# Performance work log

Hardware: AMD Instinct MI355X
Metric: run time of the kernel (lower is better)

The kernel has to match this reference:

```python
import jax, jax.numpy as jnp
import numpy as np

FEATURE_HEIGHT = 50
FEATURE_WIDTH = 50


def setup_inputs() -> dict:
    key = jax.random.key(0)
    k1, k2, k3 = jax.random.split(key, 3)
    bs, K, H, D = 16, FEATURE_HEIGHT * FEATURE_WIDTH, 8, 32
    Q, L, P = 2000, 1, 4
    value = jax.random.normal(k1, (bs, K, H, D), dtype=jnp.float32)
    value_spatial_shapes = jnp.array([[FEATURE_HEIGHT, FEATURE_WIDTH]], dtype=jnp.int64)
    sampling_locations = jax.random.uniform(k2, (bs, Q, H, L, P, 2), dtype=jnp.float32)
    attention_weights = jax.random.uniform(k3, (bs, Q, H, L, P), dtype=jnp.float32)
    return {
        "value": value,
        "value_spatial_shapes": value_spatial_shapes,
        "sampling_locations": sampling_locations,
        "attention_weights": attention_weights,
    }


def _bilinear_sample(img, grid):
    """torch.F.grid_sample(mode='bilinear', padding_mode='zeros', align_corners=False).

    img:  (N, D, h, w)
    grid: (N, Q, P, 2), last dim (x, y) in [-1, 1]
    returns (N, D, Q, P)
    """
    N, D, h, w = img.shape
    # unnormalize (align_corners=False)
    x = (grid[..., 0] + 1.0) * (w * 0.5) - 0.5  # (N, Q, P)
    y = (grid[..., 1] + 1.0) * (h * 0.5) - 0.5
    x0 = jnp.floor(x)
    y0 = jnp.floor(y)
    x1 = x0 + 1.0
    y1 = y0 + 1.0
    wx1 = x - x0
    wx0 = 1.0 - wx1
    wy1 = y - y0
    wy0 = 1.0 - wy1

    img_flat = img.reshape(N, D, h * w)

    def corner(ix, iy, wgt):
        valid = ((ix >= 0) & (ix < w) & (iy >= 0) & (iy < h)).astype(img.dtype)
        ixc = jnp.clip(ix, 0, w - 1).astype(jnp.int32)
        iyc = jnp.clip(iy, 0, h - 1).astype(jnp.int32)
        idx = (iyc * w + ixc).reshape(N, -1)  # (N, Q*P)
        vals = jnp.take_along_axis(img_flat, idx[:, None, :], axis=2)  # (N, D, Q*P)
        vals = vals.reshape(N, D, *ix.shape[1:])  # (N, D, Q, P)
        return vals * (wgt * valid)[:, None]

    out = corner(x0, y0, wx0 * wy0)
    out = out + corner(x1, y0, wx1 * wy0)
    out = out + corner(x0, y1, wx0 * wy1)
    out = out + corner(x1, y1, wx1 * wy1)
    return out


def reference(value, value_spatial_shapes, sampling_locations, attention_weights):
    bs, K, H, D = value.shape
    _, Q, _, L, P, _ = sampling_locations.shape
    h, w = FEATURE_HEIGHT, FEATURE_WIDTH

    sampling_grids = 2.0 * sampling_locations - 1.0  # (bs, Q, H, L, P, 2)
    # value -> (bs*H, D, h, w)
    v = value.reshape(bs, K, H * D).transpose(0, 2, 1).reshape(bs * H, D, h, w)
    # level 0 grid -> (bs*H, Q, P, 2)
    g = jnp.transpose(sampling_grids[:, :, :, 0], (0, 2, 1, 3, 4)).reshape(bs * H, Q, P, 2)
    sampled = _bilinear_sample(v, g)  # (bs*H, D, Q, P)
    # attention weights -> (bs*H, 1, Q, L*P)
    aw = jnp.transpose(attention_weights, (0, 2, 1, 3, 4)).reshape(bs * H, 1, Q, L * P)
    out = (sampled * aw).sum(-1)  # (bs*H, D, Q)
    out = out.reshape(bs, H * D, Q).transpose(0, 2, 1)  # (bs, Q, H*D)
    return out
```

## Files before the change

kernel.cpp:

```cpp
#include <hip/hip_runtime.h>


#define FH 50
#define FW 50
#define KK (FH * FW)
#define NH 8
#define ND 32
#define NQ 2000
#define NP 4
#define TPB 1024
#define QSLOTS (TPB / 4)
#define NPASS ((NQ + QSLOTS - 1) / QSLOTS)

typedef float f32x4 __attribute__((ext_vector_type(4)));

__global__ __launch_bounds__(TPB, 4) void deform_attn_kernel(
    const float* __restrict__ value,
    const float* __restrict__ loc,
    const float* __restrict__ attw,
    float* __restrict__ out)
{
    const int id = blockIdx.x;
    const int half = id >> 7;
    const int bh = id & 127;
    const int b  = bh >> 3;
    const int h  = bh & 7;

    __shared__ f32x4 lds[KK * 4];

    const int t = threadIdx.x;

    {
        const f32x4* __restrict__ src =
            (const f32x4*)value + (size_t)b * KK * 64 + h * 8 + half * 4;
#pragma unroll
        for (int i = 0; i < (KK * 4 + TPB - 1) / TPB; ++i) {
            const int idx = i * TPB + t;
            if (idx < KK * 4) {
                const int k = idx >> 2;
                const int q = idx & 3;
                lds[idx] = src[(size_t)k * 64 + q];
            }
        }
    }
    __syncthreads();

    const int quad = t & 3;
    const int qi = t >> 2;

    const f32x4* __restrict__ lp = (const f32x4*)loc;
    const f32x4* __restrict__ ap = (const f32x4*)attw;
    f32x4* __restrict__ op = (f32x4*)out;

    for (int pass = 0; pass < NPASS; ++pass) {
        const int qq = pass * QSLOTS + qi;
        if (qq >= NQ) break;

        const int gid = (b * NQ + qq) * NH + h;
        const f32x4 l0 = lp[(size_t)gid * 2 + 0];
        const f32x4 l1 = lp[(size_t)gid * 2 + 1];
        const f32x4 a4 = ap[gid];

        const float pxx[NP] = {l0.x, l0.z, l1.x, l1.z};
        const float pyy[NP] = {l0.y, l0.w, l1.y, l1.w};
        const float awp[NP] = {a4.x, a4.y, a4.z, a4.w};

        int   idx[16];
        float wts[16];
#pragma unroll
        for (int p = 0; p < NP; ++p) {
            const float fx = pxx[p] * (float)FW - 0.5f;
            const float fy = pyy[p] * (float)FH - 0.5f;
            const float x0f = floorf(fx);
            const float y0f = floorf(fy);
            const int x0 = (int)x0f, y0 = (int)y0f;
            const int x1 = x0 + 1, y1 = y0 + 1;
            const float wx1 = fx - x0f, wx0 = 1.f - wx1;
            const float wy1 = fy - y0f, wy0 = 1.f - wy1;

            const bool vx0 = (x0 >= 0) & (x0 < FW);
            const bool vx1 = (x1 >= 0) & (x1 < FW);
            const bool vy0 = (y0 >= 0) & (y0 < FH);
            const bool vy1 = (y1 >= 0) & (y1 < FH);

            const int cx0 = min(max(x0, 0), FW - 1);
            const int cx1 = min(max(x1, 0), FW - 1);
            const int cy0 = min(max(y0, 0), FH - 1);
            const int cy1 = min(max(y1, 0), FH - 1);

            idx[p * 4 + 0] = cy0 * FW + cx0;
            idx[p * 4 + 1] = cy0 * FW + cx1;
            idx[p * 4 + 2] = cy1 * FW + cx0;
            idx[p * 4 + 3] = cy1 * FW + cx1;

            wts[p * 4 + 0] = ((vx0 & vy0) ? (wx0 * wy0) : 0.f) * awp[p];
            wts[p * 4 + 1] = ((vx1 & vy0) ? (wx1 * wy0) : 0.f) * awp[p];
            wts[p * 4 + 2] = ((vx0 & vy1) ? (wx0 * wy1) : 0.f) * awp[p];
            wts[p * 4 + 3] = ((vx1 & vy1) ? (wx1 * wy1) : 0.f) * awp[p];
        }

        f32x4 acc = {0.f, 0.f, 0.f, 0.f};
#pragma unroll
        for (int i = 0; i < 16; ++i) {
            const f32x4 v = lds[idx[i] * 4 + quad];
            acc.x += wts[i] * v.x;
            acc.y += wts[i] * v.y;
            acc.z += wts[i] * v.z;
            acc.w += wts[i] * v.w;
        }

        op[(size_t)(b * NQ + qq) * 64 + h * 8 + half * 4 + quad] = acc;
    }
}

extern "C" void kernel_launch(void* const* d_in, const int* in_sizes, int n_in,
                              void* d_out, int out_size, void* d_ws, size_t ws_size,
                              hipStream_t stream) {
    const float* value = (const float*)d_in[0];
    const float* loc  = (const float*)d_in[2];
    const float* attw = (const float*)d_in[3];
    float* out = (float*)d_out;

    const int blocks = 2 * 16 * 8;
    deform_attn_kernel<<<blocks, TPB, 0, stream>>>(value, loc, attw, out);
}
```

Baseline: 115.6 us.

## Software-pipeline query loads and weight computation ahead of LDS gathers

```diff
diff --git a/kernel.cpp b/kernel.cpp
--- a/kernel.cpp
+++ b/kernel.cpp
@@ -10,7 +10,7 @@
 #define NP 4
 #define TPB 1024
 #define QSLOTS (TPB / 4)
-#define NPASS ((NQ + QSLOTS - 1) / QSLOTS)
+#define NPASS 8
 
 typedef float f32x4 __attribute__((ext_vector_type(4)));
 
@@ -29,44 +29,35 @@
     __shared__ f32x4 lds[KK * 4];
 
     const int t = threadIdx.x;
+    const int quad = t & 3;
+    const int qi = t >> 2;
+
+    const f32x4* __restrict__ lp = (const f32x4*)loc;
+    const f32x4* __restrict__ ap = (const f32x4*)attw;
+
+    const int gid0 = (b * NQ + qi) * NH + h;
+    f32x4 nl0 = lp[(size_t)gid0 * 2 + 0];
+    f32x4 nl1 = lp[(size_t)gid0 * 2 + 1];
+    f32x4 na  = ap[gid0];
 
     {
         const f32x4* __restrict__ src =
             (const f32x4*)value + (size_t)b * KK * 64 + h * 8 + half * 4;
 #pragma unroll
-        for (int i = 0; i < (KK * 4 + TPB - 1) / TPB; ++i) {
-            const int idx = i * TPB + t;
-            if (idx < KK * 4) {
-                const int k = idx >> 2;
-                const int q = idx & 3;
-                lds[idx] = src[(size_t)k * 64 + q];
-            }
+        for (int i = 0; i < 10; ++i) {
+            const int j = i * TPB + t;
+            if (j < KK * 4)
+                lds[j] = src[(size_t)(j >> 2) * 64 + (j & 3)];
         }
     }
-    __syncthreads();
 
-    const int quad = t & 3;
-    const int qi = t >> 2;
+    int   idx[16];
+    float wts[16];
 
-    const f32x4* __restrict__ lp = (const f32x4*)loc;
-    const f32x4* __restrict__ ap = (const f32x4*)attw;
-    f32x4* __restrict__ op = (f32x4*)out;
-
-    for (int pass = 0; pass < NPASS; ++pass) {
-        const int qq = pass * QSLOTS + qi;
-        if (qq >= NQ) break;
-
-        const int gid = (b * NQ + qq) * NH + h;
-        const f32x4 l0 = lp[(size_t)gid * 2 + 0];
-        const f32x4 l1 = lp[(size_t)gid * 2 + 1];
-        const f32x4 a4 = ap[gid];
-
+    auto computeOW = [&](const f32x4 l0, const f32x4 l1, const f32x4 a4) {
         const float pxx[NP] = {l0.x, l0.z, l1.x, l1.z};
         const float pyy[NP] = {l0.y, l0.w, l1.y, l1.w};
         const float awp[NP] = {a4.x, a4.y, a4.z, a4.w};
-
-        int   idx[16];
-        float wts[16];
 #pragma unroll
         for (int p = 0; p < NP; ++p) {
             const float fx = pxx[p] * (float)FW - 0.5f;
@@ -98,18 +89,56 @@
             wts[p * 4 + 2] = ((vx0 & vy1) ? (wx0 * wy1) : 0.f) * awp[p];
             wts[p * 4 + 3] = ((vx1 & vy1) ? (wx1 * wy1) : 0.f) * awp[p];
         }
+    };
 
-        f32x4 acc = {0.f, 0.f, 0.f, 0.f};
+    {
+        const f32x4 cl0 = nl0, cl1 = nl1, ca = na;
+        const int qn = qi + QSLOTS;
+        const int gidn = (b * NQ + qn) * NH + h;
+        nl0 = lp[(size_t)gidn * 2 + 0];
+        nl1 = lp[(size_t)gidn * 2 + 1];
+        na  = ap[gidn];
+        computeOW(cl0, cl1, ca);
+    }
+
+    __syncthreads();
+
+    f32x4* __restrict__ op = (f32x4*)out;
+
+#pragma unroll 1
+    for (int pass = 0; pass < NPASS; ++pass) {
+        const int qq = pass * QSLOTS + qi;
+
+        if (qq < NQ) {
+            f32x4 v[16];
 #pragma unroll
-        for (int i = 0; i < 16; ++i) {
-            const f32x4 v = lds[idx[i] * 4 + quad];
-            acc.x += wts[i] * v.x;
-            acc.y += wts[i] * v.y;
-            acc.z += wts[i] * v.z;
-            acc.w += wts[i] * v.w;
+            for (int i = 0; i < 16; ++i)
+                v[i] = lds[idx[i] * 4 + quad];
+            asm volatile("" ::
+                "v"(v[0]), "v"(v[1]), "v"(v[2]), "v"(v[3]),
+                "v"(v[4]), "v"(v[5]), "v"(v[6]), "v"(v[7]),
+                "v"(v[8]), "v"(v[9]), "v"(v[10]), "v"(v[11]),
+                "v"(v[12]), "v"(v[13]), "v"(v[14]), "v"(v[15]));
+            f32x4 acc = {0.f, 0.f, 0.f, 0.f};
+#pragma unroll
+            for (int i = 0; i < 16; ++i) {
+                acc.x += wts[i] * v[i].x;
+                acc.y += wts[i] * v[i].y;
+                acc.z += wts[i] * v[i].z;
+                acc.w += wts[i] * v[i].w;
+            }
+            op[(size_t)(b * NQ + qq) * 64 + h * 8 + half * 4 + quad] = acc;
         }
 
-        op[(size_t)(b * NQ + qq) * 64 + h * 8 + half * 4 + quad] = acc;
+        if (pass < NPASS - 1) {
+            const f32x4 cl0 = nl0, cl1 = nl1, ca = na;
+            const int qn = min(qq + 2 * QSLOTS, NQ - 1);
+            const int gidn = (b * NQ + qn) * NH + h;
+            nl0 = lp[(size_t)gidn * 2 + 0];
+            nl1 = lp[(size_t)gidn * 2 + 1];
+            na  = ap[gidn];
+            computeOW(cl0, cl1, ca);
+        }
     }
 }
 
```

Result: no change. 117.5 us (+1.7%).

## Map one query per thread with swizzled LDS, prefetch locations, XCD-aware block order

Applied to the files above, without the earlier changes.

```diff
diff --git a/kernel.cpp b/kernel.cpp
--- a/kernel.cpp
+++ b/kernel.cpp
@@ -9,10 +9,12 @@
 #define NQ 2000
 #define NP 4
 #define TPB 1024
-#define QSLOTS (TPB / 4)
-#define NPASS ((NQ + QSLOTS - 1) / QSLOTS)
 
 typedef float f32x4 __attribute__((ext_vector_type(4)));
+
+__device__ __forceinline__ int swz16(int k, int q) {
+    return (k << 2) ^ (q ^ (k & 3)) ^ (k & 4);
+}
 
 __global__ __launch_bounds__(TPB, 4) void deform_attn_kernel(
     const float* __restrict__ value,
@@ -20,53 +22,53 @@
     const float* __restrict__ attw,
     float* __restrict__ out)
 {
-    const int id = blockIdx.x;
-    const int half = id >> 7;
-    const int bh = id & 127;
-    const int b  = bh >> 3;
-    const int h  = bh & 7;
+    const int n = blockIdx.x;
+    const int xcd = n & 7;
+    const int slot = n >> 3;
+    const int b = xcd + ((slot >> 4) << 3);
+    const int rem = slot & 15;
+    const int h = rem >> 1;
+    const int half = rem & 1;
 
     __shared__ f32x4 lds[KK * 4];
 
     const int t = threadIdx.x;
 
+    const f32x4* __restrict__ lp = (const f32x4*)loc;
+    const f32x4* __restrict__ ap = (const f32x4*)attw;
+
+    const int gid0 = (b * NQ + t) * NH + h;
+    f32x4 l0A = lp[(size_t)gid0 * 2 + 0];
+    f32x4 l1A = lp[(size_t)gid0 * 2 + 1];
+    f32x4 aA  = ap[gid0];
+
     {
         const f32x4* __restrict__ src =
             (const f32x4*)value + (size_t)b * KK * 64 + h * 8 + half * 4;
 #pragma unroll
-        for (int i = 0; i < (KK * 4 + TPB - 1) / TPB; ++i) {
-            const int idx = i * TPB + t;
-            if (idx < KK * 4) {
-                const int k = idx >> 2;
-                const int q = idx & 3;
-                lds[idx] = src[(size_t)k * 64 + q];
+        for (int i = 0; i < 10; ++i) {
+            const int j = i * TPB + t;
+            if (j < KK * 4) {
+                const int k = j >> 2, q = j & 3;
+                lds[swz16(k, q)] = src[(size_t)k * 64 + q];
             }
         }
     }
-    __syncthreads();
 
-    const int quad = t & 3;
-    const int qi = t >> 2;
+    const int q1 = TPB + t;
+    const bool act1 = (q1 < NQ);
+    const int gid1 = (b * NQ + min(q1, NQ - 1)) * NH + h;
+    f32x4 l0B = lp[(size_t)gid1 * 2 + 0];
+    f32x4 l1B = lp[(size_t)gid1 * 2 + 1];
+    f32x4 aB  = ap[gid1];
 
-    const f32x4* __restrict__ lp = (const f32x4*)loc;
-    const f32x4* __restrict__ ap = (const f32x4*)attw;
-    f32x4* __restrict__ op = (f32x4*)out;
+    int   a16[16];
+    float wts[16];
 
-    for (int pass = 0; pass < NPASS; ++pass) {
-        const int qq = pass * QSLOTS + qi;
-        if (qq >= NQ) break;
-
-        const int gid = (b * NQ + qq) * NH + h;
-        const f32x4 l0 = lp[(size_t)gid * 2 + 0];
-        const f32x4 l1 = lp[(size_t)gid * 2 + 1];
-        const f32x4 a4 = ap[gid];
-
+    auto computeOW = [&](const f32x4 l0, const f32x4 l1, const f32x4 a4) {
         const float pxx[NP] = {l0.x, l0.z, l1.x, l1.z};
         const float pyy[NP] = {l0.y, l0.w, l1.y, l1.w};
         const float awp[NP] = {a4.x, a4.y, a4.z, a4.w};
-
-        int   idx[16];
-        float wts[16];
 #pragma unroll
         for (int p = 0; p < NP; ++p) {
             const float fx = pxx[p] * (float)FW - 0.5f;
@@ -88,28 +90,60 @@
             const int cy0 = min(max(y0, 0), FH - 1);
             const int cy1 = min(max(y1, 0), FH - 1);
 
-            idx[p * 4 + 0] = cy0 * FW + cx0;
-            idx[p * 4 + 1] = cy0 * FW + cx1;
-            idx[p * 4 + 2] = cy1 * FW + cx0;
-            idx[p * 4 + 3] = cy1 * FW + cx1;
+            const int k00 = cy0 * FW + cx0;
+            const int k01 = cy0 * FW + cx1;
+            const int k10 = cy1 * FW + cx0;
+            const int k11 = cy1 * FW + cx1;
+
+            a16[p * 4 + 0] = swz16(k00, 0);
+            a16[p * 4 + 1] = swz16(k01, 0);
+            a16[p * 4 + 2] = swz16(k10, 0);
+            a16[p * 4 + 3] = swz16(k11, 0);
 
             wts[p * 4 + 0] = ((vx0 & vy0) ? (wx0 * wy0) : 0.f) * awp[p];
             wts[p * 4 + 1] = ((vx1 & vy0) ? (wx1 * wy0) : 0.f) * awp[p];
             wts[p * 4 + 2] = ((vx0 & vy1) ? (wx0 * wy1) : 0.f) * awp[p];
             wts[p * 4 + 3] = ((vx1 & vy1) ? (wx1 * wy1) : 0.f) * awp[p];
         }
+    };
 
-        f32x4 acc = {0.f, 0.f, 0.f, 0.f};
+    f32x4* __restrict__ op = (f32x4*)out;
+
+    auto gatherStore = [&](int q) {
+        f32x4 acc0 = {0.f, 0.f, 0.f, 0.f};
+        f32x4 acc1 = {0.f, 0.f, 0.f, 0.f};
+        f32x4 acc2 = {0.f, 0.f, 0.f, 0.f};
+        f32x4 acc3 = {0.f, 0.f, 0.f, 0.f};
 #pragma unroll
-        for (int i = 0; i < 16; ++i) {
-            const f32x4 v = lds[idx[i] * 4 + quad];
-            acc.x += wts[i] * v.x;
-            acc.y += wts[i] * v.y;
-            acc.z += wts[i] * v.z;
-            acc.w += wts[i] * v.w;
+        for (int i = 0; i < 16; i += 2) {
+            f32x4 v[8];
+#pragma unroll
+            for (int j = 0; j < 2; ++j)
+#pragma unroll
+                for (int qd = 0; qd < 4; ++qd)
+                    v[j * 4 + qd] = lds[a16[i + j] ^ qd];
+            asm volatile("" ::
+                "v"(v[0]), "v"(v[1]), "v"(v[2]), "v"(v[3]),
+                "v"(v[4]), "v"(v[5]), "v"(v[6]), "v"(v[7]));
+            const float w0 = wts[i], w1 = wts[i + 1];
+            acc0 += w0 * v[0];  acc1 += w0 * v[1];
+            acc2 += w0 * v[2];  acc3 += w0 * v[3];
+            acc0 += w1 * v[4];  acc1 += w1 * v[5];
+            acc2 += w1 * v[6];  acc3 += w1 * v[7];
         }
+        f32x4* o = op + (size_t)(b * NQ + q) * 64 + h * 8 + half * 4;
+        o[0] = acc0; o[1] = acc1; o[2] = acc2; o[3] = acc3;
+    };
 
-        op[(size_t)(b * NQ + qq) * 64 + h * 8 + half * 4 + quad] = acc;
+    computeOW(l0A, l1A, aA);
+
+    __syncthreads();
+
+    gatherStore(t);
+
+    if (act1) {
+        computeOW(l0B, l1B, aB);
+        gatherStore(q1);
     }
 }
 
```

Measured after the change: 118.0 us. 2.1% more time.
